# Performance work log

Hardware: AMD Instinct MI355X
Metric: run time of the kernel (lower is better)

The kernel has to match this reference:

```python
import jax, jax.numpy as jnp
import numpy as np

N_NODES = 500000
N_EDGES = 8000000
CONSTRAINT_WEIGHT = 0.1
CORRECTION_FACTOR = 0.1


def setup_inputs() -> dict:
    key = jax.random.key(0)
    k1, k2, k3 = jax.random.split(key, 3)
    pos = jax.random.normal(k1, (N_NODES, 3), dtype=jnp.float32) * 5.0
    edge_index = jax.random.randint(k2, (2, N_EDGES), 0, N_NODES, dtype=jnp.int64)
    bond_types = jax.random.randint(k3, (N_EDGES,), 0, 5, dtype=jnp.int64)
    # buffer: canonical bond lengths for types 0..4
    target_lengths = jnp.array([1.54, 1.34, 1.20, 1.40, 1.47], dtype=jnp.float32)
    # learnable per-type adjustment, init ones*0.01
    length_adjustment = jnp.ones((5,), dtype=jnp.float32) * 0.01
    return {
        "pos": pos,
        "edge_index": edge_index,
        "bond_types": bond_types,
        "target_lengths": target_lengths,
        "length_adjustment": length_adjustment,
    }


def reference(pos, edge_index, bond_types, target_lengths, length_adjustment):
    row, col = edge_index[0], edge_index[1]
    # gather endpoints, bond vectors [E,3]
    bond_vectors = pos[row] - pos[col]
    current_lengths = jnp.linalg.norm(bond_vectors, axis=-1, keepdims=True)  # [E,1]
    current_lengths = jnp.maximum(current_lengths, 1e-6)
    # per-bond-type target length with learnable adjustment
    bt = jnp.clip(bond_types, 0, 4)
    tgt = (target_lengths[bt] + length_adjustment[bt])[:, None]  # [E,1]
    length_errors = jnp.abs(current_lengths - tgt)
    constraint_loss = jnp.mean(length_errors) * CONSTRAINT_WEIGHT
    # soft constraint: nudge positions toward target length
    length_ratio = jnp.clip(tgt / current_lengths, 0.8, 1.2)
    # adjustment = (bond_vectors*ratio - bond_vectors) * correction_factor
    adjustment = bond_vectors * (length_ratio - 1.0) * CORRECTION_FACTOR  # [E,3]
    half = adjustment * 0.5
    pos_new = pos.at[row].add(half).at[col].add(-half)
    return pos_new, constraint_loss
```

## Files before the change

kernel.cpp:

```cpp
#include <hip/hip_runtime.h>
#include <math.h>

#define N_NODES 500000
#define N_EDGES 8000000
#define N3 (N_NODES * 3)
#define N3_4 (N3 / 4)
#define CONSTRAINT_WEIGHT 0.1f
#define CORRECTION_FACTOR 0.1f

#define WBITS 11
#define WSZ (1 << WBITS)
#define NWIN 245
#define WFL (WSZ * 3)
#define NB 256
#define BT 512

typedef unsigned long long u64;
typedef unsigned int u32;

__device__ __forceinline__ unsigned short f2bf(float f) {
    u32 u = __float_as_uint(f);
    return (unsigned short)((u + 0x7FFFu + ((u >> 16) & 1u)) >> 16);
}
__device__ __forceinline__ float bf2f(u32 h) { return __uint_as_float(h << 16); }

__global__ void zero_kernel(int* __restrict__ p, int n_ints) {
    int stride = gridDim.x * blockDim.x;
    for (int i = blockIdx.x * blockDim.x + threadIdx.x; i < n_ints; i += stride)
        p[i] = 0;
}

__global__ void copy_kernel(const float4* __restrict__ pos4, float4* __restrict__ out4) {
    int stride = gridDim.x * blockDim.x;
    for (int i = blockIdx.x * blockDim.x + threadIdx.x; i < N3_4; i += stride)
        out4[i] = pos4[i];
}

__global__ __launch_bounds__(BT) void count_kernel(const int* __restrict__ eidx,
                                                   int e0, int e1,
                                                   int* __restrict__ bcnt) {
    __shared__ int s_hist[NWIN];
    int tid = threadIdx.x;
    for (int w = tid; w < NWIN; w += BT) s_hist[w] = 0;
    __syncthreads();

    int total = e1 - e0;
    int chunk = (total + NB - 1) / NB;
    int es = e0 + blockIdx.x * chunk;
    int ee = es + chunk; if (ee > e1) ee = e1;

    for (int e = es + tid; e < ee; e += BT) {
        atomicAdd(&s_hist[eidx[e] >> WBITS], 1);
        atomicAdd(&s_hist[eidx[N_EDGES + e] >> WBITS], 1);
    }
    __syncthreads();
    int* row = bcnt + (size_t)blockIdx.x * NWIN;
    for (int w = tid; w < NWIN; w += BT) row[w] = s_hist[w];
}

__global__ __launch_bounds__(NB) void prefix_kernel(int* __restrict__ bcnt,
                                                    int* __restrict__ counts) {
    __shared__ int s[NB];
    int w = blockIdx.x, b = threadIdx.x;
    int v = bcnt[(size_t)b * NWIN + w];
    s[b] = v;
    __syncthreads();
    for (int off = 1; off < NB; off <<= 1) {
        int t = (b >= off) ? s[b - off] : 0;
        __syncthreads();
        s[b] += t;
        __syncthreads();
    }
    bcnt[(size_t)b * NWIN + w] = s[b] - v;
    if (b == NB - 1) counts[w] = s[b];
}

__global__ __launch_bounds__(BT) void emit_kernel(
        const int* __restrict__ eidx, const int* __restrict__ btype,
        const float* __restrict__ tl, const float* __restrict__ la,
        const float* __restrict__ pos,
        const int* __restrict__ bcnt, u64* __restrict__ buf, int cap,
        int e0, int e1, double* __restrict__ acc) {
    __shared__ int s_base[NWIN];
    __shared__ int s_cur[NWIN];
    __shared__ float s_tgt[5];
    __shared__ float warp_sums[BT / 64];
    int tid = threadIdx.x;
    if (tid < 5) s_tgt[tid] = tl[tid] + la[tid];
    const int* row = bcnt + (size_t)blockIdx.x * NWIN;
    for (int w = tid; w < NWIN; w += BT) { s_base[w] = row[w]; s_cur[w] = 0; }
    __syncthreads();

    int total = e1 - e0;
    int chunk = (total + NB - 1) / NB;
    int es = e0 + blockIdx.x * chunk;
    int ee = es + chunk; if (ee > e1) ee = e1;

    float lsum = 0.0f;
    for (int e = es + tid; e < ee; e += BT) {
        int r = eidx[e];
        int c = eidx[N_EDGES + e];
        int bt = btype[e]; bt = min(max(bt, 0), 4);
        float tgt = s_tgt[bt];
        float ax = pos[3 * r], ay = pos[3 * r + 1], az = pos[3 * r + 2];
        float bx = pos[3 * c], by = pos[3 * c + 1], bz = pos[3 * c + 2];
        float dx = ax - bx, dy = ay - by, dz = az - bz;
        float len = fmaxf(sqrtf(dx * dx + dy * dy + dz * dz), 1e-6f);
        lsum += fabsf(len - tgt);
        float ratio = fminf(fmaxf(tgt / len, 0.8f), 1.2f);
        float s = (ratio - 1.0f) * (CORRECTION_FACTOR * 0.5f);
        float hx = dx * s, hy = dy * s, hz = dz * s;
        {
            int w = r >> WBITS;
            int slot = s_base[w] + atomicAdd(&s_cur[w], 1);
            if (slot < cap) {
                u64 rec = (u64)(r & (WSZ - 1)) | ((u64)f2bf(hx) << 16)
                        | ((u64)f2bf(hy) << 32) | ((u64)f2bf(hz) << 48);
                buf[(size_t)w * cap + slot] = rec;
            }
        }
        {
            int w = c >> WBITS;
            int slot = s_base[w] + atomicAdd(&s_cur[w], 1);
            if (slot < cap) {
                u64 rec = (u64)(c & (WSZ - 1)) | ((u64)f2bf(-hx) << 16)
                        | ((u64)f2bf(-hy) << 32) | ((u64)f2bf(-hz) << 48);
                buf[(size_t)w * cap + slot] = rec;
            }
        }
    }

    for (int off = 32; off; off >>= 1)
        lsum += __shfl_down(lsum, off, 64);
    int wid = tid >> 6, lane = tid & 63;
    if (lane == 0) warp_sums[wid] = lsum;
    __syncthreads();
    if (tid == 0) {
        float bsum = 0.0f;
        for (int w = 0; w < BT / 64; ++w) bsum += warp_sums[w];
        atomicAdd(acc, (double)bsum);
    }
}

__global__ __launch_bounds__(256) void accum_kernel(const u64* __restrict__ buf,
                                                    const int* __restrict__ counts, int cap,
                                                    float* __restrict__ delta) {
    __shared__ float facc[WFL];
    int w = blockIdx.x, tid = threadIdx.x;
    for (int i = tid; i < WFL; i += 256) facc[i] = 0.0f;
    __syncthreads();
    int n = counts[w]; if (n > cap) n = cap; if (n < 0) n = 0;
    const u64* b = buf + (size_t)w * cap;
    for (int i = tid; i < n; i += 256) {
        u64 rec = b[i];
        int lid = (int)(rec & (u64)(WSZ - 1));
        atomicAdd(&facc[lid * 3 + 0], bf2f((u32)((rec >> 16) & 0xFFFF)));
        atomicAdd(&facc[lid * 3 + 1], bf2f((u32)((rec >> 32) & 0xFFFF)));
        atomicAdd(&facc[lid * 3 + 2], bf2f((u32)(rec >> 48)));
    }
    __syncthreads();
    float* d = delta + (size_t)w * WFL;
    for (int i = tid; i < WFL; i += 256) d[i] += facc[i];
}

__global__ void merge_kernel(const float4* __restrict__ pos4,
                             const float4* __restrict__ delta4,
                             float4* __restrict__ out4) {
    int stride = gridDim.x * blockDim.x;
    for (int i = blockIdx.x * blockDim.x + threadIdx.x; i < N3_4; i += stride) {
        float4 p = pos4[i], d = delta4[i];
        p.x += d.x; p.y += d.y; p.z += d.z; p.w += d.w;
        out4[i] = p;
    }
}

__global__ void finalize_kernel(const double* __restrict__ acc,
                                float* __restrict__ out_loss) {
    *out_loss = (float)(*acc / (double)N_EDGES * (double)CONSTRAINT_WEIGHT);
}


__global__ void copy_init_kernel(const float4* __restrict__ pos4,
                                 float4* __restrict__ out4,
                                 int n4, double* __restrict__ acc) {
    int i = blockIdx.x * blockDim.x + threadIdx.x;
    if (i == 0) *acc = 0.0;
    int stride = gridDim.x * blockDim.x;
    for (int k = i; k < n4; k += stride)
        out4[k] = pos4[k];
}

__global__ void edge_kernel_direct(const float* __restrict__ pos,
                                   const int* __restrict__ eidx,
                                   const int* __restrict__ btype,
                                   const float* __restrict__ tl,
                                   const float* __restrict__ la,
                                   float* __restrict__ out_pos,
                                   double* __restrict__ acc) {
    __shared__ float s_tgt[5];
    if (threadIdx.x < 5) s_tgt[threadIdx.x] = tl[threadIdx.x] + la[threadIdx.x];
    __syncthreads();
    float lsum = 0.0f;
    int stride = gridDim.x * blockDim.x;
    for (int e = blockIdx.x * blockDim.x + threadIdx.x; e < N_EDGES; e += stride) {
        int r = eidx[e];
        int c = eidx[N_EDGES + e];
        int bt = btype[e]; bt = min(max(bt, 0), 4);
        float tgt = s_tgt[bt];
        float ax = pos[3 * r], ay = pos[3 * r + 1], az = pos[3 * r + 2];
        float bx = pos[3 * c], by = pos[3 * c + 1], bz = pos[3 * c + 2];
        float dx = ax - bx, dy = ay - by, dz = az - bz;
        float len = fmaxf(sqrtf(dx * dx + dy * dy + dz * dz), 1e-6f);
        lsum += fabsf(len - tgt);
        float ratio = fminf(fmaxf(tgt / len, 0.8f), 1.2f);
        float s = (ratio - 1.0f) * (CORRECTION_FACTOR * 0.5f);
        float hx = dx * s, hy = dy * s, hz = dz * s;
        atomicAdd(&out_pos[3 * r],     hx);
        atomicAdd(&out_pos[3 * r + 1], hy);
        atomicAdd(&out_pos[3 * r + 2], hz);
        atomicAdd(&out_pos[3 * c],    -hx);
        atomicAdd(&out_pos[3 * c + 1], -hy);
        atomicAdd(&out_pos[3 * c + 2], -hz);
    }
    for (int off = 32; off; off >>= 1)
        lsum += __shfl_down(lsum, off, 64);
    __shared__ float warp_sums[16];
    int wid = threadIdx.x >> 6, lane = threadIdx.x & 63;
    if (lane == 0) warp_sums[wid] = lsum;
    __syncthreads();
    if (threadIdx.x == 0) {
        float bsum = 0.0f;
        int nw = blockDim.x >> 6;
        for (int w = 0; w < nw; ++w) bsum += warp_sums[w];
        atomicAdd(acc, (double)bsum);
    }
}

extern "C" void kernel_launch(void* const* d_in, const int* in_sizes, int n_in,
                              void* d_out, int out_size, void* d_ws, size_t ws_size,
                              hipStream_t stream) {
    const float* pos   = (const float*)d_in[0];
    const int*   eidx  = (const int*)d_in[1];
    const int*   btype = (const int*)d_in[2];
    const float* tl    = (const float*)d_in[3];
    const float* la    = (const float*)d_in[4];
    float* out = (float*)d_out;

    const size_t off_delta  = 16;
    const size_t delta_bytes = (size_t)NWIN * WFL * 4;
    const size_t off_bcnt   = off_delta + delta_bytes;
    const size_t off_counts = off_bcnt + (size_t)NB * NWIN * 4;
    const size_t off_buf    = (off_counts + (size_t)NWIN * 4 + 15) & ~(size_t)15;

    int P = 0, cap = 0;
    const int pcand[5] = {1, 2, 4, 8, 16};
    for (int k = 0; k < 5; ++k) {
        int p = pcand[k];
        long epp = (N_EDGES + p - 1) / p;
        double m = 2.0 * (double)epp * WSZ / (double)N_NODES;
        int c = (int)(m + 8.0 * sqrt(m) + 64.0);
        c = (c + 7) & ~7;
        size_t need = off_buf + (size_t)NWIN * (size_t)c * 8;
        if (need <= ws_size) { P = p; cap = c; break; }
    }

    if (P) {
        double* acc  = (double*)d_ws;
        float* delta = (float*)((char*)d_ws + off_delta);
        int*   bcnt  = (int*)((char*)d_ws + off_bcnt);
        int*   cnts  = (int*)((char*)d_ws + off_counts);
        u64*   buf   = (u64*)((char*)d_ws + off_buf);

        zero_kernel<<<1024, 256, 0, stream>>>((int*)d_ws, (int)(off_bcnt / 4));
        copy_kernel<<<1024, 256, 0, stream>>>((const float4*)pos, (float4*)out);
        int epp = (N_EDGES + P - 1) / P;
        for (int p = 0; p < P; ++p) {
            int e0 = p * epp;
            int e1 = e0 + epp; if (e1 > N_EDGES) e1 = N_EDGES;
            if (e0 >= e1) break;
            count_kernel<<<NB, BT, 0, stream>>>(eidx, e0, e1, bcnt);
            prefix_kernel<<<NWIN, NB, 0, stream>>>(bcnt, cnts);
            emit_kernel<<<NB, BT, 0, stream>>>(eidx, btype, tl, la, pos,
                                               bcnt, buf, cap, e0, e1, acc);
            accum_kernel<<<NWIN, 256, 0, stream>>>(buf, cnts, cap, delta);
        }
        merge_kernel<<<1024, 256, 0, stream>>>((const float4*)pos, (const float4*)delta,
                                               (float4*)out);
        finalize_kernel<<<1, 1, 0, stream>>>(acc, out + N3);
    } else {
        double* acc = (double*)d_ws;
        copy_init_kernel<<<1024, 256, 0, stream>>>((const float4*)pos, (float4*)out, N3_4, acc);
        edge_kernel_direct<<<4096, 256, 0, stream>>>(pos, eidx, btype, tl, la, out, acc);
        finalize_kernel<<<1, 1, 0, stream>>>(acc, out + N3);
    }
}
```

Baseline: 746.2 us.

## Fuse window accumulation with position merge and add nontemporal edge streaming

For the single-pass case, a new kernel accumulates each window's bf16 deltas in shared memory and writes pos+delta straight to the output. This removes the separate copy, delta zeroing, delta write-back and merge passes. It also raises the block count for the count/emit partition from 256 to 1024 and switches edge-index, bond-type and record-buffer accesses to nontemporal loads and stores. The per-window capacity slack drops from 8 to 6 standard deviations, which shrinks the buffer but makes overflow drops more likely on skewed inputs.

```diff
diff --git a/kernel.cpp b/kernel.cpp
--- a/kernel.cpp
+++ b/kernel.cpp
@@ -12,7 +12,7 @@
 #define WSZ (1 << WBITS)
 #define NWIN 245
 #define WFL (WSZ * 3)
-#define NB 256
+#define NB 1024
 #define BT 512
 
 typedef unsigned long long u64;
@@ -28,12 +28,6 @@
     int stride = gridDim.x * blockDim.x;
     for (int i = blockIdx.x * blockDim.x + threadIdx.x; i < n_ints; i += stride)
         p[i] = 0;
-}
-
-__global__ void copy_kernel(const float4* __restrict__ pos4, float4* __restrict__ out4) {
-    int stride = gridDim.x * blockDim.x;
-    for (int i = blockIdx.x * blockDim.x + threadIdx.x; i < N3_4; i += stride)
-        out4[i] = pos4[i];
 }
 
 __global__ __launch_bounds__(BT) void count_kernel(const int* __restrict__ eidx,
@@ -50,8 +44,10 @@
     int ee = es + chunk; if (ee > e1) ee = e1;
 
     for (int e = es + tid; e < ee; e += BT) {
-        atomicAdd(&s_hist[eidx[e] >> WBITS], 1);
-        atomicAdd(&s_hist[eidx[N_EDGES + e] >> WBITS], 1);
+        int r = __builtin_nontemporal_load(&eidx[e]);
+        int c = __builtin_nontemporal_load(&eidx[N_EDGES + e]);
+        atomicAdd(&s_hist[r >> WBITS], 1);
+        atomicAdd(&s_hist[c >> WBITS], 1);
     }
     __syncthreads();
     int* row = bcnt + (size_t)blockIdx.x * NWIN;
@@ -98,9 +94,10 @@
 
     float lsum = 0.0f;
     for (int e = es + tid; e < ee; e += BT) {
-        int r = eidx[e];
-        int c = eidx[N_EDGES + e];
-        int bt = btype[e]; bt = min(max(bt, 0), 4);
+        int r = __builtin_nontemporal_load(&eidx[e]);
+        int c = __builtin_nontemporal_load(&eidx[N_EDGES + e]);
+        int bt = __builtin_nontemporal_load(&btype[e]);
+        bt = min(max(bt, 0), 4);
         float tgt = s_tgt[bt];
         float ax = pos[3 * r], ay = pos[3 * r + 1], az = pos[3 * r + 2];
         float bx = pos[3 * c], by = pos[3 * c + 1], bz = pos[3 * c + 2];
@@ -116,7 +113,7 @@
             if (slot < cap) {
                 u64 rec = (u64)(r & (WSZ - 1)) | ((u64)f2bf(hx) << 16)
                         | ((u64)f2bf(hy) << 32) | ((u64)f2bf(hz) << 48);
-                buf[(size_t)w * cap + slot] = rec;
+                __builtin_nontemporal_store(rec, &buf[(size_t)w * cap + slot]);
             }
         }
         {
@@ -125,7 +122,7 @@
             if (slot < cap) {
                 u64 rec = (u64)(c & (WSZ - 1)) | ((u64)f2bf(-hx) << 16)
                         | ((u64)f2bf(-hy) << 32) | ((u64)f2bf(-hz) << 48);
-                buf[(size_t)w * cap + slot] = rec;
+                __builtin_nontemporal_store(rec, &buf[(size_t)w * cap + slot]);
             }
         }
     }
@@ -139,6 +136,34 @@
         float bsum = 0.0f;
         for (int w = 0; w < BT / 64; ++w) bsum += warp_sums[w];
         atomicAdd(acc, (double)bsum);
+    }
+}
+
+__global__ __launch_bounds__(512) void accum_fused_kernel(
+        const u64* __restrict__ buf, const int* __restrict__ counts, int cap,
+        const float4* __restrict__ pos4, float4* __restrict__ out4) {
+    __shared__ __align__(16) float facc[WFL];
+    int w = blockIdx.x, tid = threadIdx.x;
+    for (int i = tid; i < WFL; i += 512) facc[i] = 0.0f;
+    __syncthreads();
+    int n = counts[w]; if (n > cap) n = cap; if (n < 0) n = 0;
+    const u64* b = buf + (size_t)w * cap;
+    for (int i = tid; i < n; i += 512) {
+        u64 rec = __builtin_nontemporal_load(&b[i]);
+        int lid = (int)(rec & (u64)(WSZ - 1));
+        atomicAdd(&facc[lid * 3 + 0], bf2f((u32)((rec >> 16) & 0xFFFF)));
+        atomicAdd(&facc[lid * 3 + 1], bf2f((u32)((rec >> 32) & 0xFFFF)));
+        atomicAdd(&facc[lid * 3 + 2], bf2f((u32)(rec >> 48)));
+    }
+    __syncthreads();
+    const float4* f4 = (const float4*)facc;
+    int base4 = w * (WFL / 4);
+    int lim4 = (N3 - w * WFL) / 4;
+    if (lim4 > WFL / 4) lim4 = WFL / 4;
+    for (int i = tid; i < lim4; i += 512) {
+        float4 p = pos4[base4 + i], d = f4[i];
+        p.x += d.x; p.y += d.y; p.z += d.z; p.w += d.w;
+        out4[base4 + i] = p;
     }
 }
 
@@ -258,13 +283,27 @@
         int p = pcand[k];
         long epp = (N_EDGES + p - 1) / p;
         double m = 2.0 * (double)epp * WSZ / (double)N_NODES;
-        int c = (int)(m + 8.0 * sqrt(m) + 64.0);
+        int c = (int)(m + 6.0 * sqrt(m) + 64.0);
         c = (c + 7) & ~7;
         size_t need = off_buf + (size_t)NWIN * (size_t)c * 8;
         if (need <= ws_size) { P = p; cap = c; break; }
     }
 
-    if (P) {
+    if (P == 1) {
+        double* acc  = (double*)d_ws;
+        int*   bcnt  = (int*)((char*)d_ws + off_bcnt);
+        int*   cnts  = (int*)((char*)d_ws + off_counts);
+        u64*   buf   = (u64*)((char*)d_ws + off_buf);
+
+        zero_kernel<<<1, 64, 0, stream>>>((int*)d_ws, 4);
+        count_kernel<<<NB, BT, 0, stream>>>(eidx, 0, N_EDGES, bcnt);
+        prefix_kernel<<<NWIN, NB, 0, stream>>>(bcnt, cnts);
+        emit_kernel<<<NB, BT, 0, stream>>>(eidx, btype, tl, la, pos,
+                                           bcnt, buf, cap, 0, N_EDGES, acc);
+        accum_fused_kernel<<<NWIN, 512, 0, stream>>>(buf, cnts, cap,
+                                                     (const float4*)pos, (float4*)out);
+        finalize_kernel<<<1, 1, 0, stream>>>(acc, out + N3);
+    } else if (P) {
         double* acc  = (double*)d_ws;
         float* delta = (float*)((char*)d_ws + off_delta);
         int*   bcnt  = (int*)((char*)d_ws + off_bcnt);
@@ -272,7 +311,6 @@
         u64*   buf   = (u64*)((char*)d_ws + off_buf);
 
         zero_kernel<<<1024, 256, 0, stream>>>((int*)d_ws, (int)(off_bcnt / 4));
-        copy_kernel<<<1024, 256, 0, stream>>>((const float4*)pos, (float4*)out);
         int epp = (N_EDGES + P - 1) / P;
         for (int p = 0; p < P; ++p) {
             int e0 = p * epp;
```

Result: slower. 1.071 ms (+43.6%).
